# Optimization experiments

Measured on AMD Instinct MI355X. Metric: run time of the kernel, lower is better.

Reference implementation:

```python
import jax, jax.numpy as jnp
import numpy as np

B, T, F = 8192, 200, 16
H = 32  # LSTM units
D = 60  # 6 * FREQUENCY


def setup_inputs() -> dict:
    key = jax.random.key(0)
    ks = jax.random.split(key, 5)
    s = 0.1
    return {
        "x": jax.random.normal(ks[0], (B, T, F), jnp.float32),
        "W": jax.random.normal(ks[1], (F, 4 * H), jnp.float32) * s,
        "U": jax.random.normal(ks[2], (H, 4 * H), jnp.float32) * s,
        "b": jnp.zeros((4 * H,), jnp.float32),
        "W1": jax.random.normal(ks[3], (H, D), jnp.float32) * s,
        "b1": jnp.zeros((D,), jnp.float32),
        "W2": jax.random.normal(ks[4], (H, D), jnp.float32) * s,
        "b2": jnp.zeros((D,), jnp.float32),
    }


def _lstm_last(x, W, U, b):
    # Precompute input-to-gate projections for all timesteps: [B, T, 4H]
    xg = jnp.einsum('btf,fg->btg', x, W) + b
    batch = x.shape[0]
    h0 = jnp.zeros((batch, H), x.dtype)
    c0 = jnp.zeros((batch, H), x.dtype)

    def step(carry, xg_t):
        h, c = carry
        g = xg_t + h @ U  # [B, 4H]
        i, f, cc, o = jnp.split(g, 4, axis=-1)  # Keras gate order: i, f, c, o
        i = jax.nn.sigmoid(i)
        f = jax.nn.sigmoid(f)
        o = jax.nn.sigmoid(o)
        c_new = f * c + i * jax.nn.relu(cc)  # activation=relu
        h_new = o * jax.nn.relu(c_new)
        return (h_new, c_new), None

    (h_T, _), _ = jax.lax.scan(step, (h0, c0), jnp.swapaxes(xg, 0, 1))
    return h_T  # return_sequences=False -> last hidden state [B, H]


def reference(x, W, U, b, W1, b1, W2, b2):
    h = _lstm_last(x, W, U, b)
    long_pred = h @ W1 + b1
    lat_pred = h @ W2 + b2
    return (long_pred, lat_pred)
```

## Files before the change

kernel.cpp:

```cpp
#include <hip/hip_runtime.h>

#define BATCH 8192
#define TSTEPS 200
#define FEAT 16
#define HID 32
#define GATES 128
#define DOUT 60
#define ROWS 16
#define HSTRIDE 40

typedef __fp16 half2v __attribute__((ext_vector_type(2)));
typedef __fp16 half4v __attribute__((ext_vector_type(4)));
typedef __fp16 half8v __attribute__((ext_vector_type(8)));
typedef float  float2v __attribute__((ext_vector_type(2)));
typedef float  float4v __attribute__((ext_vector_type(4)));

__device__ __forceinline__ half2v pkrtz(float a, float b) {
    return __builtin_amdgcn_cvt_pkrtz(a, b);
}

__device__ __forceinline__ half4v pack4(float4 v) {
    half2v lo = pkrtz(v.x, v.y);
    half2v hi = pkrtz(v.z, v.w);
    half4v r;
    r[0] = lo[0]; r[1] = lo[1]; r[2] = hi[0]; r[3] = hi[1];
    return r;
}

__device__ __forceinline__ void lds_barrier() {
    __builtin_amdgcn_sched_barrier(0);
    asm volatile("s_waitcnt lgkmcnt(0)\n\ts_barrier" ::: "memory");
    __builtin_amdgcn_sched_barrier(0);
}

template <bool DO_XW, bool DO_LOAD, int LOFF>
__device__ __forceinline__ void lstm_step(
    float4& XN, const float* xp,
    const half8v (&aU)[4], const half4v (&aW)[4], const float4v (&bias)[4],
    float4v (&accx)[4], float2v (&cst)[2],
    const __fp16* hr, __fp16* hw, int hroff, int hwoff)
{
    half8v hB = *reinterpret_cast<const half8v*>(&hr[hroff]);

    float4v acc[4];
    #pragma unroll
    for (int tt = 0; tt < 4; tt++)
        acc[tt] = __builtin_amdgcn_mfma_f32_16x16x32_f16(
            aU[tt], hB, accx[tt], 0, 0, 0);

    if (DO_XW) {
        half4v ax = pack4(XN);
        #pragma unroll
        for (int tt = 0; tt < 4; tt++)
            accx[tt] = __builtin_amdgcn_mfma_f32_16x16x16f16(
                aW[tt], ax, bias[tt], 0, 0, 0);
    }
    if (DO_LOAD)
        XN = *reinterpret_cast<const float4*>(xp + LOFF);

    const float2v one  = {1.0f, 1.0f};
    const float2v zero = {0.0f, 0.0f};
    union { half4v v; half2v h2[2]; } hv;
    #pragma unroll
    for (int p = 0; p < 2; p++) {
        float2v ei, ef, eo;
        ei[0] = __builtin_amdgcn_exp2f(acc[0][2 * p]);
        ei[1] = __builtin_amdgcn_exp2f(acc[0][2 * p + 1]);
        ef[0] = __builtin_amdgcn_exp2f(acc[1][2 * p]);
        ef[1] = __builtin_amdgcn_exp2f(acc[1][2 * p + 1]);
        eo[0] = __builtin_amdgcn_exp2f(acc[3][2 * p]);
        eo[1] = __builtin_amdgcn_exp2f(acc[3][2 * p + 1]);
        float2v di  = one + ei;
        float2v df  = one + ef;
        float2v dov = one + eo;
        float2v cc2 = {acc[2][2 * p], acc[2][2 * p + 1]};
        float2v rc  = __builtin_elementwise_max(cc2, zero);
        float2v num = __builtin_elementwise_fma(cst[p], di, rc * df);
        float2v ee  = (di * df) * dov;
        float   Q   = __builtin_amdgcn_rcpf(ee[0] * ee[1]);
        float2v ie  = {Q * ee[1], Q * ee[0]};
        float2v c2  = num * (ie * dov);
        cst[p] = c2;
        float2v h2  = __builtin_elementwise_max(num, zero) * ie;
        hv.h2[p] = pkrtz(h2[0], h2[1]);
    }
    *reinterpret_cast<half4v*>(&hw[hwoff]) = hv.v;
    lds_barrier();
}

__global__ __launch_bounds__(128, 1) void lstm_mfma(
    const float* __restrict__ x,
    const float* __restrict__ W,
    const float* __restrict__ U,
    const float* __restrict__ bg,
    const float* __restrict__ W1,
    const float* __restrict__ b1,
    const float* __restrict__ W2,
    const float* __restrict__ b2,
    float* __restrict__ out)
{
    const int tid  = threadIdx.x;
    const int lane = tid & 63;
    const int w    = tid >> 6;
    const int n16  = lane & 15;
    const int g    = lane >> 4;
    const int b0   = blockIdx.x * ROWS;

    __shared__ __align__(16) __fp16 hbuf[2][ROWS * HSTRIDE];

    half8v  aU[4];
    half4v  aW[4];
    float4v bias[4];
    #pragma unroll
    for (int tt = 0; tt < 4; tt++) {
        const float s = (tt == 2) ? 1.0f : -1.44269504088896340736f;
        const int colA = 32 * tt + 16 * w + n16;
        half8v u8;
        #pragma unroll
        for (int j = 0; j < 8; j++)
            u8[j] = (__fp16)(U[(8 * g + j) * GATES + colA] * s);
        aU[tt] = u8;
        half4v w4;
        #pragma unroll
        for (int j = 0; j < 4; j++)
            w4[j] = (__fp16)(W[(4 * g + j) * GATES + colA] * s);
        aW[tt] = w4;
        float4v bv;
        #pragma unroll
        for (int r = 0; r < 4; r++)
            bv[r] = bg[32 * tt + 16 * w + 4 * g + r] * s;
        bias[tt] = bv;
    }

    for (int i = tid; i < ROWS * HSTRIDE; i += 128) hbuf[0][i] = (__fp16)0.f;

    const float* xrow = x + (size_t)(b0 + n16) * TSTEPS * FEAT + 4 * g;

    float4 xf0 = *reinterpret_cast<const float4*>(xrow + FEAT);
    float4 xf1 = *reinterpret_cast<const float4*>(xrow + 2 * FEAT);

    float4v accx[4];
    {
        half4v a0 = pack4(*reinterpret_cast<const float4*>(xrow));
        #pragma unroll
        for (int tt = 0; tt < 4; tt++)
            accx[tt] = __builtin_amdgcn_mfma_f32_16x16x16f16(
                aW[tt], a0, bias[tt], 0, 0, 0);
    }

    float2v cst[2] = {{0.f, 0.f}, {0.f, 0.f}};
    const int hroff = n16 * HSTRIDE + 8 * g;
    const int hwoff = n16 * HSTRIDE + 16 * w + 4 * g;

    __syncthreads();

    const float* xp = xrow;
    for (int it = 0; it < (TSTEPS - 4) / 2; ++it) {
        lstm_step<true, true, 3 * FEAT>(xf0, xp, aU, aW, bias, accx, cst,
                                        hbuf[0], hbuf[1], hroff, hwoff);
        lstm_step<true, true, 4 * FEAT>(xf1, xp, aU, aW, bias, accx, cst,
                                        hbuf[1], hbuf[0], hroff, hwoff);
        xp += 2 * FEAT;
    }
    lstm_step<true, true, 3 * FEAT>(xf0, xp, aU, aW, bias, accx, cst,
                                    hbuf[0], hbuf[1], hroff, hwoff);
    lstm_step<true, false, 0>(xf1, xp, aU, aW, bias, accx, cst,
                              hbuf[1], hbuf[0], hroff, hwoff);
    lstm_step<true, false, 0>(xf0, xp, aU, aW, bias, accx, cst,
                              hbuf[0], hbuf[1], hroff, hwoff);
    lstm_step<false, false, 0>(xf1, xp, aU, aW, bias, accx, cst,
                               hbuf[1], hbuf[0], hroff, hwoff);

    const __fp16* hf = &hbuf[0][0];
    for (int idx = tid; idx < ROWS * DOUT; idx += 128) {
        const int row = idx / DOUT;
        const int d   = idx - row * DOUT;
        float s1 = b1[d], s2 = b2[d];
        #pragma unroll 8
        for (int k = 0; k < HID; k++) {
            float hv = (float)hf[row * HSTRIDE + k];
            s1 = fmaf(hv, W1[k * DOUT + d], s1);
            s2 = fmaf(hv, W2[k * DOUT + d], s2);
        }
        out[(size_t)(b0 + row) * DOUT + d] = s1;
        out[(size_t)BATCH * DOUT + (size_t)(b0 + row) * DOUT + d] = s2;
    }
}

extern "C" void kernel_launch(void* const* d_in, const int* in_sizes, int n_in,
                              void* d_out, int out_size, void* d_ws, size_t ws_size,
                              hipStream_t stream) {
    const float* x  = (const float*)d_in[0];
    const float* W  = (const float*)d_in[1];
    const float* U  = (const float*)d_in[2];
    const float* bg = (const float*)d_in[3];
    const float* W1 = (const float*)d_in[4];
    const float* b1 = (const float*)d_in[5];
    const float* W2 = (const float*)d_in[6];
    const float* b2 = (const float*)d_in[7];
    float* out = (float*)d_out;

    dim3 grid(BATCH / ROWS);
    dim3 block(128);
    lstm_mfma<<<grid, block, 0, stream>>>(x, W, U, bg, W1, b1, W2, b2, out);
}
```

Before: 235.1 us.

## Split LSTM gate work across four waves per 16-row block

Doubles the workgroup from two to four waves. Each wave now owns 8 hidden units instead of 16, which halves the per-wave MFMA and elementwise gate work on each recurrent step. The gate columns are permuted so that each wave's two MFMA tiles carry the i/f and c/o gates for matching hidden units, keeping the nonlinearity local to a lane. The aim is to shorten the serial per-timestep critical path, at the cost of more waves taking part in each LDS barrier and every wave redundantly reloading x.

```diff
diff --git a/kernel.cpp b/kernel.cpp
--- a/kernel.cpp
+++ b/kernel.cpp
@@ -8,6 +8,7 @@
 #define DOUT 60
 #define ROWS 16
 #define HSTRIDE 40
+#define NL2E -1.44269504088896340736f
 
 typedef __fp16 half2v __attribute__((ext_vector_type(2)));
 typedef __fp16 half4v __attribute__((ext_vector_type(4)));
@@ -36,59 +37,54 @@
 template <bool DO_XW, bool DO_LOAD, int LOFF>
 __device__ __forceinline__ void lstm_step(
     float4& XN, const float* xp,
-    const half8v (&aU)[4], const half4v (&aW)[4], const float4v (&bias)[4],
-    float4v (&accx)[4], float2v (&cst)[2],
+    const half8v (&aU)[2], const half4v (&aW)[2], const float4v (&bias)[2],
+    float4v (&accx)[2], float2v& cst,
     const __fp16* hr, __fp16* hw, int hroff, int hwoff)
 {
     half8v hB = *reinterpret_cast<const half8v*>(&hr[hroff]);
 
-    float4v acc[4];
-    #pragma unroll
-    for (int tt = 0; tt < 4; tt++)
-        acc[tt] = __builtin_amdgcn_mfma_f32_16x16x32_f16(
-            aU[tt], hB, accx[tt], 0, 0, 0);
+    float4v acc0 = __builtin_amdgcn_mfma_f32_16x16x32_f16(
+        aU[0], hB, accx[0], 0, 0, 0);
+    float4v acc1 = __builtin_amdgcn_mfma_f32_16x16x32_f16(
+        aU[1], hB, accx[1], 0, 0, 0);
 
     if (DO_XW) {
         half4v ax = pack4(XN);
-        #pragma unroll
-        for (int tt = 0; tt < 4; tt++)
-            accx[tt] = __builtin_amdgcn_mfma_f32_16x16x16f16(
-                aW[tt], ax, bias[tt], 0, 0, 0);
+        accx[0] = __builtin_amdgcn_mfma_f32_16x16x16f16(
+            aW[0], ax, bias[0], 0, 0, 0);
+        accx[1] = __builtin_amdgcn_mfma_f32_16x16x16f16(
+            aW[1], ax, bias[1], 0, 0, 0);
     }
     if (DO_LOAD)
         XN = *reinterpret_cast<const float4*>(xp + LOFF);
 
     const float2v one  = {1.0f, 1.0f};
     const float2v zero = {0.0f, 0.0f};
-    union { half4v v; half2v h2[2]; } hv;
-    #pragma unroll
-    for (int p = 0; p < 2; p++) {
-        float2v ei, ef, eo;
-        ei[0] = __builtin_amdgcn_exp2f(acc[0][2 * p]);
-        ei[1] = __builtin_amdgcn_exp2f(acc[0][2 * p + 1]);
-        ef[0] = __builtin_amdgcn_exp2f(acc[1][2 * p]);
-        ef[1] = __builtin_amdgcn_exp2f(acc[1][2 * p + 1]);
-        eo[0] = __builtin_amdgcn_exp2f(acc[3][2 * p]);
-        eo[1] = __builtin_amdgcn_exp2f(acc[3][2 * p + 1]);
-        float2v di  = one + ei;
-        float2v df  = one + ef;
-        float2v dov = one + eo;
-        float2v cc2 = {acc[2][2 * p], acc[2][2 * p + 1]};
-        float2v rc  = __builtin_elementwise_max(cc2, zero);
-        float2v num = __builtin_elementwise_fma(cst[p], di, rc * df);
-        float2v ee  = (di * df) * dov;
-        float   Q   = __builtin_amdgcn_rcpf(ee[0] * ee[1]);
-        float2v ie  = {Q * ee[1], Q * ee[0]};
-        float2v c2  = num * (ie * dov);
-        cst[p] = c2;
-        float2v h2  = __builtin_elementwise_max(num, zero) * ie;
-        hv.h2[p] = pkrtz(h2[0], h2[1]);
-    }
-    *reinterpret_cast<half4v*>(&hw[hwoff]) = hv.v;
+    float2v ei, ef, eo;
+    ei[0] = __builtin_amdgcn_exp2f(acc0[0]);
+    ei[1] = __builtin_amdgcn_exp2f(acc0[1]);
+    ef[0] = __builtin_amdgcn_exp2f(acc0[2]);
+    ef[1] = __builtin_amdgcn_exp2f(acc0[3]);
+    eo[0] = __builtin_amdgcn_exp2f(acc1[2]);
+    eo[1] = __builtin_amdgcn_exp2f(acc1[3]);
+    float2v di  = one + ei;
+    float2v df  = one + ef;
+    float2v dov = one + eo;
+    float2v cc2 = {acc1[0], acc1[1]};
+    float2v rc  = __builtin_elementwise_max(cc2, zero);
+    float2v num = __builtin_elementwise_fma(cst, di, rc * df);
+    float2v ee  = (di * df) * dov;
+    float   Q   = __builtin_amdgcn_rcpf(ee[0] * ee[1]);
+    float2v ie  = {Q * ee[1], Q * ee[0]};
+    float2v c2  = num * (ie * dov);
+    cst = c2;
+    float2v h2  = __builtin_elementwise_max(num, zero) * ie;
+    *reinterpret_cast<half2v*>(&hw[hwoff]) = pkrtz(h2[0], h2[1]);
+
     lds_barrier();
 }
 
-__global__ __launch_bounds__(128, 1) void lstm_mfma(
+__global__ __launch_bounds__(256, 1) void lstm_mfma(
     const float* __restrict__ x,
     const float* __restrict__ W,
     const float* __restrict__ U,
@@ -108,49 +104,53 @@
 
     __shared__ __align__(16) __fp16 hbuf[2][ROWS * HSTRIDE];
 
-    half8v  aU[4];
-    half4v  aW[4];
-    float4v bias[4];
+    half8v  aU[2];
+    half4v  aW[2];
+    float4v bias[2];
     #pragma unroll
-    for (int tt = 0; tt < 4; tt++) {
-        const float s = (tt == 2) ? 1.0f : -1.44269504088896340736f;
-        const int colA = 32 * tt + 16 * w + n16;
+    for (int tt2 = 0; tt2 < 2; tt2++) {
+        const int gA   = 2 * tt2 + ((n16 >> 1) & 1);
+        const float sA = (gA == 2) ? 1.0f : NL2E;
+        const int colA = 32 * gA + 8 * w + 2 * (n16 >> 2) + (n16 & 1);
         half8v u8;
         #pragma unroll
         for (int j = 0; j < 8; j++)
-            u8[j] = (__fp16)(U[(8 * g + j) * GATES + colA] * s);
-        aU[tt] = u8;
+            u8[j] = (__fp16)(U[(8 * g + j) * GATES + colA] * sA);
+        aU[tt2] = u8;
         half4v w4;
         #pragma unroll
         for (int j = 0; j < 4; j++)
-            w4[j] = (__fp16)(W[(4 * g + j) * GATES + colA] * s);
-        aW[tt] = w4;
+            w4[j] = (__fp16)(W[(4 * g + j) * GATES + colA] * sA);
+        aW[tt2] = w4;
         float4v bv;
         #pragma unroll
-        for (int r = 0; r < 4; r++)
-            bv[r] = bg[32 * tt + 16 * w + 4 * g + r] * s;
-        bias[tt] = bv;
-    }
-
-    for (int i = tid; i < ROWS * HSTRIDE; i += 128) hbuf[0][i] = (__fp16)0.f;
+        for (int r = 0; r < 4; r++) {
+            const int gi = 2 * tt2 + (r >> 1);
+            const int cb = 32 * gi + 8 * w + 2 * g + (r & 1);
+            bv[r] = bg[cb] * ((gi == 2) ? 1.0f : NL2E);
+        }
+        bias[tt2] = bv;
+    }
+
+    for (int i = tid; i < ROWS * HSTRIDE; i += 256) hbuf[0][i] = (__fp16)0.f;
 
     const float* xrow = x + (size_t)(b0 + n16) * TSTEPS * FEAT + 4 * g;
 
     float4 xf0 = *reinterpret_cast<const float4*>(xrow + FEAT);
     float4 xf1 = *reinterpret_cast<const float4*>(xrow + 2 * FEAT);
 
-    float4v accx[4];
+    float4v accx[2];
     {
         half4v a0 = pack4(*reinterpret_cast<const float4*>(xrow));
-        #pragma unroll
-        for (int tt = 0; tt < 4; tt++)
-            accx[tt] = __builtin_amdgcn_mfma_f32_16x16x16f16(
-                aW[tt], a0, bias[tt], 0, 0, 0);
-    }
-
-    float2v cst[2] = {{0.f, 0.f}, {0.f, 0.f}};
+        accx[0] = __builtin_amdgcn_mfma_f32_16x16x16f16(
+            aW[0], a0, bias[0], 0, 0, 0);
+        accx[1] = __builtin_amdgcn_mfma_f32_16x16x16f16(
+            aW[1], a0, bias[1], 0, 0, 0);
+    }
+
+    float2v cst = {0.f, 0.f};
     const int hroff = n16 * HSTRIDE + 8 * g;
-    const int hwoff = n16 * HSTRIDE + 16 * w + 4 * g;
+    const int hwoff = n16 * HSTRIDE + 8 * w + 2 * g;
 
     __syncthreads();
 
@@ -172,7 +172,7 @@
                                hbuf[1], hbuf[0], hroff, hwoff);
 
     const __fp16* hf = &hbuf[0][0];
-    for (int idx = tid; idx < ROWS * DOUT; idx += 128) {
+    for (int idx = tid; idx < ROWS * DOUT; idx += 256) {
         const int row = idx / DOUT;
         const int d   = idx - row * DOUT;
         float s1 = b1[d], s2 = b2[d];
@@ -201,6 +201,6 @@
     float* out = (float*)d_out;
 
     dim3 grid(BATCH / ROWS);
-    dim3 block(128);
+    dim3 block(256);
     lstm_mfma<<<grid, block, 0, stream>>>(x, W, U, bg, W1, b1, W2, b2, out);
 }
```

New measurement: 210.0 us. -10.7%, faster.
